# Performance work log

Measured on AMD Instinct MI355X. Metric: run time of the kernel, lower is better.

## Reference

```python
import jax, jax.numpy as jnp
import numpy as np

H = 1024   # hidden_size
IN = 512   # input_size
B = 256    # batch
T = 256    # timesteps

DT = 0.1
DELTA_T = 1.0
Z_MIN = 0.001
Z_MAX = 0.1


def setup_inputs() -> dict:
    key = jax.random.key(0)
    ks = jax.random.split(key, 10)
    bound = 1.0 / np.sqrt(H)
    u = lambda k, shape: jax.random.uniform(k, shape, jnp.float32, -bound, bound)
    return {
        "x":   jax.random.normal(ks[0], (T, IN, B), jnp.float32),
        "c_x": u(ks[1], (H, 1)),
        "c_u": u(ks[2], (H, 1)),
        "c_U": u(ks[3], (H, 1)),
        "w_r": u(ks[4], (H, H)),
        "p_r": u(ks[5], (H, IN)),
        "b_r": u(ks[6], (H, 1)),
        "g_z": u(ks[7], (H, 1)),
        "K":   u(ks[8], (H, H)),
        "p_z": u(ks[9], (H, IN)),
    }


def reference(x, c_x, c_u, c_U, w_r, p_r, b_r, g_z, K, p_z):
    # Gate-rate constants (computed once; they don't depend on state)
    z_x = Z_MIN + (Z_MAX - Z_MIN) * jax.nn.sigmoid(c_x)   # (H,1)
    z_u = Z_MIN + (Z_MAX - Z_MIN) * jax.nn.sigmoid(c_u)   # (H,1)
    Ucap = 0.9 * jax.nn.sigmoid(c_U)                      # (H,1)
    Ucap_sg = jax.lax.stop_gradient(Ucap)                 # clamp bound is detached in torch

    def step(carry, xt):
        X, U, v = carry                   # each (H,B); xt: (IN,B)
        r = jax.nn.sigmoid(v)             # r_t from previous v_t
        X_new = z_x + (1.0 - z_x) * X - DELTA_T * U * X * r
        U_new = Ucap * z_u + (1.0 - z_u) * U + DELTA_T * Ucap * (1.0 - U) * r
        U_new = jnp.clip(U_new, Ucap_sg, 1.0)
        z_t = DT * jax.nn.sigmoid(K @ r + p_z @ xt + g_z)
        v_new = (1.0 - z_t) * v + DT * (w_r @ (U_new * X_new * r) + p_r @ xt + b_r)
        return (X_new, U_new, v_new), v_new

    X0 = jnp.ones((H, B), jnp.float32)
    U0 = jnp.full((H, B), 0.9, jnp.float32)
    v0 = jnp.zeros((H, B), jnp.float32)

    (_, _, _), vs = jax.lax.scan(step, (X0, U0, v0), x)
    # return hidden-state trajectory as (T, batch, hidden)
    return jnp.transpose(vs, (0, 2, 1))
```

## Files before the change

### kernel.cpp

```cpp
#include <hip/hip_runtime.h>
#include <hip/hip_bf16.h>

#define Hh 1024
#define INs 512
#define Bb 256
#define Tt 256
#define DT_ 0.1f
#define Z_MIN_ 0.001f
#define Z_MAX_ 0.1f
#define KW (Hh + INs)
#define NB 256

typedef __attribute__((ext_vector_type(8))) short short8;
typedef __attribute__((ext_vector_type(4))) float f32x4;
typedef __attribute__((ext_vector_type(2))) float f32x2;

__device__ __forceinline__ float sigmoidf_(float x) {
    return 1.0f / (1.0f + __expf(-x));
}

__device__ __forceinline__ unsigned short f2bf(float f) {
    union { float f; unsigned u; } v; v.f = f;
    unsigned r = v.u + 0x7FFFu + ((v.u >> 16) & 1u);
    return (unsigned short)(r >> 16);
}

__global__ __launch_bounds__(256) void build_weights(
    const float* __restrict__ Km, const float* __restrict__ p_z,
    const float* __restrict__ w_r, const float* __restrict__ p_r,
    unsigned short* __restrict__ W1, unsigned short* __restrict__ W2) {
    int idx = blockIdx.x * 256 + threadIdx.x;
    int h = idx / KW, k = idx % KW;
    float a = (k < Hh) ? Km[h * Hh + k] : p_z[h * INs + (k - Hh)];
    float b = (k < Hh) ? w_r[h * Hh + k] : p_r[h * INs + (k - Hh)];
    W1[idx] = f2bf(a);
    W2[idx] = f2bf(b);
}

__global__ __launch_bounds__(256) void transpose_x(
    const float* __restrict__ x, unsigned short* __restrict__ xT) {
    __shared__ unsigned short tile[64][65];
    int t = blockIdx.z;
    int i0 = blockIdx.y * 64;
    int b0 = blockIdx.x * 64;
    int c = threadIdx.x & 63, rbase = threadIdx.x >> 6;
    const float* xp = x + (size_t)t * INs * Bb;
#pragma unroll
    for (int r = 0; r < 16; ++r) {
        int row = r * 4 + rbase;
        tile[row][c] = f2bf(xp[(size_t)(i0 + row) * Bb + (b0 + c)]);
    }
    __syncthreads();
    unsigned short* op = xT + (size_t)t * Bb * INs;
#pragma unroll
    for (int r = 0; r < 16; ++r) {
        int brow = r * 4 + rbase;
        op[(size_t)(b0 + brow) * INs + (i0 + c)] = tile[c][brow];
    }
}

__global__ __launch_bounds__(256) void precomp_gates(
    const float* __restrict__ c_x, const float* __restrict__ c_u,
    const float* __restrict__ c_U,
    float* __restrict__ zxv, float* __restrict__ zuv, float* __restrict__ Ucv) {
    int h = blockIdx.x * 256 + threadIdx.x;
    zxv[h] = Z_MIN_ + (Z_MAX_ - Z_MIN_) * sigmoidf_(c_x[h]);
    zuv[h] = Z_MIN_ + (Z_MAX_ - Z_MIN_) * sigmoidf_(c_u[h]);
    Ucv[h] = 0.9f * sigmoidf_(c_U[h]);
}

__global__ __launch_bounds__(256) void init_state(
    const float* __restrict__ zxv, const float* __restrict__ zuv,
    const float* __restrict__ Ucv,
    unsigned short* __restrict__ R0, unsigned short* __restrict__ M0,
    unsigned* __restrict__ bar) {
    int idx = blockIdx.x * 256 + threadIdx.x;
    if (idx < 16) bar[idx * 32] = 0;
    int h = idx & (Hh - 1);
    float zx = zxv[h], zu = zuv[h], Uc = Ucv[h];
    const float r = 0.5f;
    float Xn = zx + (1.0f - zx) - 0.45f;
    float Un = Uc * zu + (1.0f - zu) * 0.9f + Uc * 0.05f;
    Un = fminf(fmaxf(Un, Uc), 1.0f);
    R0[idx] = f2bf(r);
    M0[idx] = f2bf(Un * Xn * r);
}

__global__ __launch_bounds__(512, 1) void persist_kernel(
    const unsigned short* __restrict__ W1, const unsigned short* __restrict__ W2,
    const unsigned short* __restrict__ xT,
    unsigned short* __restrict__ Rb0, unsigned short* __restrict__ Rb1,
    unsigned short* __restrict__ Mb0, unsigned short* __restrict__ Mb1,
    float* __restrict__ out,
    const float* __restrict__ g_z, const float* __restrict__ b_r,
    const float* __restrict__ zxv, const float* __restrict__ zuv,
    const float* __restrict__ Ucv, unsigned* __restrict__ bar) {

    const int tid = threadIdx.x;
    const int wave = tid >> 6, lane = tid & 63;
    const int m = lane & 15, q = lane >> 4;
    const int kq = wave;
    const int rowg = blockIdx.x >> 4;
    const int colg = blockIdx.x & 15;

    unsigned* cnt = bar + (unsigned)colg * 32;

    const int krec = kq * 128;
    const int kx = kq * 64;
    const int bcol = colg * 16 + m;

    short8 wf1[4][6], wf2[4][6];
#pragma unroll
    for (int rs = 0; rs < 4; ++rs) {
        const int arow = rowg * 64 + rs * 16 + m;
        const unsigned short* w1r = W1 + (size_t)arow * KW + krec + q * 8;
        const unsigned short* w2r = W2 + (size_t)arow * KW + krec + q * 8;
#pragma unroll
        for (int c = 0; c < 4; ++c) {
            wf1[rs][c] = *(const short8*)(w1r + c * 32);
            wf2[rs][c] = *(const short8*)(w2r + c * 32);
        }
        const unsigned short* w1x = W1 + (size_t)arow * KW + Hh + kx + q * 8;
        const unsigned short* w2x = W2 + (size_t)arow * KW + Hh + kx + q * 8;
#pragma unroll
        for (int c = 0; c < 2; ++c) {
            wf1[rs][4 + c] = *(const short8*)(w1x + c * 32);
            wf2[rs][4 + c] = *(const short8*)(w2x + c * 32);
        }
    }

    const int rs_e = wave >> 1, eh = wave & 1;
    const int h2 = rowg * 64 + rs_e * 16 + q * 4 + eh * 2;
    const int bcol_e = colg * 16 + m;

    f32x2 zx2 = *(const f32x2*)(zxv + h2);
    f32x2 zu2 = *(const f32x2*)(zuv + h2);
    f32x2 Uc2 = *(const f32x2*)(Ucv + h2);
    f32x2 gz2 = *(const f32x2*)(g_z + h2);
    f32x2 br2 = *(const f32x2*)(b_r + h2);

    f32x2 vr, Xr, Ur;
#pragma unroll
    for (int j = 0; j < 2; ++j) {
        vr[j] = 0.0f;
        float Xn = zx2[j] + (1.0f - zx2[j]) - 0.45f;
        float Un = Uc2[j] * zu2[j] + (1.0f - zu2[j]) * 0.9f + Uc2[j] * 0.05f;
        Un = fminf(fmaxf(Un, Uc2[j]), 1.0f);
        Xr[j] = Xn; Ur[j] = Un;
    }

    __shared__ f32x4 red[8][4][2][64];

    short8 xb[2];
    {
        const unsigned short* xp = xT + (size_t)bcol * INs + kx + q * 8;
#pragma unroll
        for (int c = 0; c < 2; ++c)
            xb[c] = *(const short8*)(xp + c * 32);
    }

    for (int t = 0; t < Tt; ++t) {
        const unsigned short* Rt = (t & 1) ? Rb1 : Rb0;
        const unsigned short* Mt = (t & 1) ? Mb1 : Mb0;
        unsigned short* Rn = (t & 1) ? Rb0 : Rb1;
        unsigned short* Mn = (t & 1) ? Mb0 : Mb1;

        f32x4 acc[4][2];
#pragma unroll
        for (int rs = 0; rs < 4; ++rs)
#pragma unroll
            for (int mt = 0; mt < 2; ++mt)
                acc[rs][mt] = (f32x4){0.0f, 0.0f, 0.0f, 0.0f};

#pragma unroll
        for (int c = 0; c < 2; ++c)
#pragma unroll
            for (int rs = 0; rs < 4; ++rs) {
                acc[rs][0] = __builtin_amdgcn_mfma_f32_16x16x32_bf16(wf1[rs][4 + c], xb[c], acc[rs][0], 0, 0, 0);
                acc[rs][1] = __builtin_amdgcn_mfma_f32_16x16x32_bf16(wf2[rs][4 + c], xb[c], acc[rs][1], 0, 0, 0);
            }

        if (t + 1 < Tt) {
            const unsigned short* xn = xT + (size_t)(t + 1) * Bb * INs
                                     + (size_t)bcol * INs + kx + q * 8;
#pragma unroll
            for (int c = 0; c < 2; ++c)
                xb[c] = *(const short8*)(xn + c * 32);
        }

        const unsigned short* rp = Rt + (size_t)bcol * Hh + krec + q * 8;
        const unsigned short* mp = Mt + (size_t)bcol * Hh + krec + q * 8;

#pragma unroll
        for (int c = 0; c < 4; ++c) {
            short8 bR = *(const short8*)(rp + c * 32);
            short8 bM = *(const short8*)(mp + c * 32);
#pragma unroll
            for (int rs = 0; rs < 4; ++rs) {
                acc[rs][0] = __builtin_amdgcn_mfma_f32_16x16x32_bf16(wf1[rs][c], bR, acc[rs][0], 0, 0, 0);
                acc[rs][1] = __builtin_amdgcn_mfma_f32_16x16x32_bf16(wf2[rs][c], bM, acc[rs][1], 0, 0, 0);
            }
        }

#pragma unroll
        for (int rs = 0; rs < 4; ++rs)
#pragma unroll
            for (int mt = 0; mt < 2; ++mt)
                red[kq][rs][mt][lane] = acc[rs][mt];
        __syncthreads();

        {
            f32x2 g1 = {0.0f, 0.0f}, g2 = {0.0f, 0.0f};
#pragma unroll
            for (int k2 = 0; k2 < 8; ++k2) {
                const float* p1 = (const float*)&red[k2][rs_e][0][lane];
                const float* p2 = (const float*)&red[k2][rs_e][1][lane];
                g1 += *(const f32x2*)(p1 + eh * 2);
                g2 += *(const f32x2*)(p2 + eh * 2);
            }

            f32x2 vv;
            ushort2 rq, mq;
#pragma unroll
            for (int j = 0; j < 2; ++j) {
                float z = DT_ * sigmoidf_(g1[j] + gz2[j]);
                float vnew = (1.0f - z) * vr[j] + DT_ * (g2[j] + br2[j]);
                vr[j] = vnew;
                vv[j] = vnew;
                float r = sigmoidf_(vnew);
                float Xs = Xr[j], Us = Ur[j];
                float Xn = zx2[j] + (1.0f - zx2[j]) * Xs - Us * Xs * r;
                float Un = Uc2[j] * zu2[j] + (1.0f - zu2[j]) * Us
                         + Uc2[j] * (1.0f - Us) * r;
                Un = fminf(fmaxf(Un, Uc2[j]), 1.0f);
                Xr[j] = Xn; Ur[j] = Un;
                unsigned short rb = f2bf(r), mb = f2bf(Un * Xn * r);
                if (j == 0) { rq.x = rb; mq.x = mb; }
                else        { rq.y = rb; mq.y = mb; }
            }
            const size_t base = (size_t)bcol_e * Hh + h2;
            *(f32x2*)(out + (size_t)t * Bb * Hh + base) = vv;
            *(ushort2*)(Rn + base) = rq;
            *(ushort2*)(Mn + base) = mq;
        }
        __syncthreads();

        if (t + 1 < Tt) {
            if (tid == 0)
                __hip_atomic_fetch_add(cnt, 1u, __ATOMIC_RELAXED,
                                       __HIP_MEMORY_SCOPE_AGENT);
            if (tid == 0) {
                const unsigned tgt = (unsigned)(t + 1) * 16u;
                while (__hip_atomic_load(cnt, __ATOMIC_RELAXED,
                                         __HIP_MEMORY_SCOPE_AGENT) < tgt)
                    __builtin_amdgcn_s_sleep(1);
                asm volatile("buffer_inv sc0" ::: "memory");
            }
            __syncthreads();
        }
    }
}

extern "C" void kernel_launch(void* const* d_in, const int* in_sizes, int n_in,
                              void* d_out, int out_size, void* d_ws, size_t ws_size,
                              hipStream_t stream) {
    const float* x   = (const float*)d_in[0];
    const float* c_x = (const float*)d_in[1];
    const float* c_u = (const float*)d_in[2];
    const float* c_U = (const float*)d_in[3];
    const float* w_r = (const float*)d_in[4];
    const float* p_r = (const float*)d_in[5];
    const float* b_r = (const float*)d_in[6];
    const float* g_z = (const float*)d_in[7];
    const float* Km  = (const float*)d_in[8];
    const float* p_z = (const float*)d_in[9];
    float* out = (float*)d_out;

    char* w = (char*)d_ws;
    unsigned short* W1 = (unsigned short*)w;   w += (size_t)Hh * KW * 2;
    unsigned short* W2 = (unsigned short*)w;   w += (size_t)Hh * KW * 2;
    unsigned short* xT = (unsigned short*)w;   w += (size_t)Tt * Bb * INs * 2;
    unsigned short* Rb0 = (unsigned short*)w;  w += (size_t)Bb * Hh * 2;
    unsigned short* Rb1 = (unsigned short*)w;  w += (size_t)Bb * Hh * 2;
    unsigned short* Mb0 = (unsigned short*)w;  w += (size_t)Bb * Hh * 2;
    unsigned short* Mb1 = (unsigned short*)w;  w += (size_t)Bb * Hh * 2;
    float* zxv = (float*)w;                    w += 4096;
    float* zuv = (float*)w;                    w += 4096;
    float* Ucv = (float*)w;                    w += 4096;
    unsigned* bar = (unsigned*)w;              w += 4096;

    build_weights<<<(Hh * KW) / 256, 256, 0, stream>>>(Km, p_z, w_r, p_r, W1, W2);
    transpose_x<<<dim3(Bb / 64, INs / 64, Tt), 256, 0, stream>>>(x, xT);
    precomp_gates<<<Hh / 256, 256, 0, stream>>>(c_x, c_u, c_U, zxv, zuv, Ucv);
    init_state<<<(Bb * Hh) / 256, 256, 0, stream>>>(zxv, zuv, Ucv, Rb0, Mb0, bar);

    persist_kernel<<<NB, 512, 0, stream>>>(
        W1, W2, xT, Rb0, Rb1, Mb0, Mb1, out,
        g_z, b_r, zxv, zuv, Ucv, bar);
}
```

Measured before the change: 1.884 ms.

## Replace atomic counter barrier with per-block byte flags and restructure epilogue

The per-column-group counter barrier built on atomic adds becomes a set of 16 byte flags, one per row group, each set with a plain atomic store. Waiters poll two 64-bit words and test with a SWAR trick that no byte still holds the old step value. This removes contended read-modify-write traffic on one counter. The R/M operand loads are also hoisted to the top of the step ahead of the x-projection MFMAs to hide latency, and the epilogue now runs on 4 waves with 4-wide vectors instead of 8 waves with 2-wide ones. The risks are that byte flags wrap after 256 steps and that a flag store may become visible before the data stores, since there is no release fence.

```diff
diff --git a/kernel.cpp b/kernel.cpp
--- a/kernel.cpp
+++ b/kernel.cpp
@@ -13,7 +13,6 @@
 
 typedef __attribute__((ext_vector_type(8))) short short8;
 typedef __attribute__((ext_vector_type(4))) float f32x4;
-typedef __attribute__((ext_vector_type(2))) float f32x2;
 
 __device__ __forceinline__ float sigmoidf_(float x) {
     return 1.0f / (1.0f + __expf(-x));
@@ -75,7 +74,7 @@
     unsigned short* __restrict__ R0, unsigned short* __restrict__ M0,
     unsigned* __restrict__ bar) {
     int idx = blockIdx.x * 256 + threadIdx.x;
-    if (idx < 16) bar[idx * 32] = 0;
+    if (idx < 512) bar[idx] = 0;
     int h = idx & (Hh - 1);
     float zx = zxv[h], zu = zuv[h], Uc = Ucv[h];
     const float r = 0.5f;
@@ -103,7 +102,7 @@
     const int rowg = blockIdx.x >> 4;
     const int colg = blockIdx.x & 15;
 
-    unsigned* cnt = bar + (unsigned)colg * 32;
+    unsigned char* flg = (unsigned char*)bar + (unsigned)colg * 128;
 
     const int krec = kq * 128;
     const int kx = kq * 64;
@@ -129,24 +128,24 @@
         }
     }
 
-    const int rs_e = wave >> 1, eh = wave & 1;
-    const int h2 = rowg * 64 + rs_e * 16 + q * 4 + eh * 2;
+    const int rs_e = wave & 3;
+    const int h04 = rowg * 64 + rs_e * 16 + q * 4;
     const int bcol_e = colg * 16 + m;
 
-    f32x2 zx2 = *(const f32x2*)(zxv + h2);
-    f32x2 zu2 = *(const f32x2*)(zuv + h2);
-    f32x2 Uc2 = *(const f32x2*)(Ucv + h2);
-    f32x2 gz2 = *(const f32x2*)(g_z + h2);
-    f32x2 br2 = *(const f32x2*)(b_r + h2);
-
-    f32x2 vr, Xr, Ur;
-#pragma unroll
-    for (int j = 0; j < 2; ++j) {
-        vr[j] = 0.0f;
-        float Xn = zx2[j] + (1.0f - zx2[j]) - 0.45f;
-        float Un = Uc2[j] * zu2[j] + (1.0f - zu2[j]) * 0.9f + Uc2[j] * 0.05f;
-        Un = fminf(fmaxf(Un, Uc2[j]), 1.0f);
-        Xr[j] = Xn; Ur[j] = Un;
+    f32x4 zx4 = *(const f32x4*)(zxv + h04);
+    f32x4 zu4 = *(const f32x4*)(zuv + h04);
+    f32x4 Uc4 = *(const f32x4*)(Ucv + h04);
+    f32x4 gz4 = *(const f32x4*)(g_z + h04);
+    f32x4 br4 = *(const f32x4*)(b_r + h04);
+
+    f32x4 vr, Xr, Ur;
+#pragma unroll
+    for (int e = 0; e < 4; ++e) {
+        vr[e] = 0.0f;
+        float Xn = zx4[e] + (1.0f - zx4[e]) - 0.45f;
+        float Un = Uc4[e] * zu4[e] + (1.0f - zu4[e]) * 0.9f + Uc4[e] * 0.05f;
+        Un = fminf(fmaxf(Un, Uc4[e]), 1.0f);
+        Xr[e] = Xn; Ur[e] = Un;
     }
 
     __shared__ f32x4 red[8][4][2][64];
@@ -165,6 +164,15 @@
         unsigned short* Rn = (t & 1) ? Rb0 : Rb1;
         unsigned short* Mn = (t & 1) ? Mb0 : Mb1;
 
+        const unsigned short* rp = Rt + (size_t)bcol * Hh + krec + q * 8;
+        const unsigned short* mp = Mt + (size_t)bcol * Hh + krec + q * 8;
+        short8 bR[4], bM[4];
+#pragma unroll
+        for (int c = 0; c < 4; ++c) {
+            bR[c] = *(const short8*)(rp + c * 32);
+            bM[c] = *(const short8*)(mp + c * 32);
+        }
+
         f32x4 acc[4][2];
 #pragma unroll
         for (int rs = 0; rs < 4; ++rs)
@@ -188,19 +196,13 @@
                 xb[c] = *(const short8*)(xn + c * 32);
         }
 
-        const unsigned short* rp = Rt + (size_t)bcol * Hh + krec + q * 8;
-        const unsigned short* mp = Mt + (size_t)bcol * Hh + krec + q * 8;
-
-#pragma unroll
-        for (int c = 0; c < 4; ++c) {
-            short8 bR = *(const short8*)(rp + c * 32);
-            short8 bM = *(const short8*)(mp + c * 32);
+#pragma unroll
+        for (int c = 0; c < 4; ++c)
 #pragma unroll
             for (int rs = 0; rs < 4; ++rs) {
-                acc[rs][0] = __builtin_amdgcn_mfma_f32_16x16x32_bf16(wf1[rs][c], bR, acc[rs][0], 0, 0, 0);
-                acc[rs][1] = __builtin_amdgcn_mfma_f32_16x16x32_bf16(wf2[rs][c], bM, acc[rs][1], 0, 0, 0);
-            }
-        }
+                acc[rs][0] = __builtin_amdgcn_mfma_f32_16x16x32_bf16(wf1[rs][c], bR[c], acc[rs][0], 0, 0, 0);
+                acc[rs][1] = __builtin_amdgcn_mfma_f32_16x16x32_bf16(wf2[rs][c], bM[c], acc[rs][1], 0, 0, 0);
+            }
 
 #pragma unroll
         for (int rs = 0; rs < 4; ++rs)
@@ -209,51 +211,63 @@
                 red[kq][rs][mt][lane] = acc[rs][mt];
         __syncthreads();
 
-        {
-            f32x2 g1 = {0.0f, 0.0f}, g2 = {0.0f, 0.0f};
-#pragma unroll
-            for (int k2 = 0; k2 < 8; ++k2) {
-                const float* p1 = (const float*)&red[k2][rs_e][0][lane];
-                const float* p2 = (const float*)&red[k2][rs_e][1][lane];
-                g1 += *(const f32x2*)(p1 + eh * 2);
-                g2 += *(const f32x2*)(p2 + eh * 2);
-            }
-
-            f32x2 vv;
-            ushort2 rq, mq;
-#pragma unroll
-            for (int j = 0; j < 2; ++j) {
-                float z = DT_ * sigmoidf_(g1[j] + gz2[j]);
-                float vnew = (1.0f - z) * vr[j] + DT_ * (g2[j] + br2[j]);
-                vr[j] = vnew;
-                vv[j] = vnew;
+        if (wave < 4) {
+            f32x4 g1 = red[0][rs_e][0][lane];
+            f32x4 g2 = red[0][rs_e][1][lane];
+#pragma unroll
+            for (int k2 = 1; k2 < 8; ++k2) {
+                g1 += red[k2][rs_e][0][lane];
+                g2 += red[k2][rs_e][1][lane];
+            }
+
+            f32x4 vv;
+            ushort4 rq, mq;
+#pragma unroll
+            for (int e = 0; e < 4; ++e) {
+                float z = DT_ * sigmoidf_(g1[e] + gz4[e]);
+                float vnew = (1.0f - z) * vr[e] + DT_ * (g2[e] + br4[e]);
+                vr[e] = vnew;
+                vv[e] = vnew;
                 float r = sigmoidf_(vnew);
-                float Xs = Xr[j], Us = Ur[j];
-                float Xn = zx2[j] + (1.0f - zx2[j]) * Xs - Us * Xs * r;
-                float Un = Uc2[j] * zu2[j] + (1.0f - zu2[j]) * Us
-                         + Uc2[j] * (1.0f - Us) * r;
-                Un = fminf(fmaxf(Un, Uc2[j]), 1.0f);
-                Xr[j] = Xn; Ur[j] = Un;
+                float Xs = Xr[e], Us = Ur[e];
+                float Xn = zx4[e] + (1.0f - zx4[e]) * Xs - Us * Xs * r;
+                float Un = Uc4[e] * zu4[e] + (1.0f - zu4[e]) * Us
+                         + Uc4[e] * (1.0f - Us) * r;
+                Un = fminf(fmaxf(Un, Uc4[e]), 1.0f);
+                Xr[e] = Xn; Ur[e] = Un;
                 unsigned short rb = f2bf(r), mb = f2bf(Un * Xn * r);
-                if (j == 0) { rq.x = rb; mq.x = mb; }
-                else        { rq.y = rb; mq.y = mb; }
-            }
-            const size_t base = (size_t)bcol_e * Hh + h2;
-            *(f32x2*)(out + (size_t)t * Bb * Hh + base) = vv;
-            *(ushort2*)(Rn + base) = rq;
-            *(ushort2*)(Mn + base) = mq;
+                if (e == 0) { rq.x = rb; mq.x = mb; }
+                else if (e == 1) { rq.y = rb; mq.y = mb; }
+                else if (e == 2) { rq.z = rb; mq.z = mb; }
+                else { rq.w = rb; mq.w = mb; }
+            }
+            const size_t base = (size_t)bcol_e * Hh + h04;
+            *(f32x4*)(out + (size_t)t * Bb * Hh + base) = vv;
+            *(ushort4*)(Rn + base) = rq;
+            *(ushort4*)(Mn + base) = mq;
         }
         __syncthreads();
 
         if (t + 1 < Tt) {
-            if (tid == 0)
-                __hip_atomic_fetch_add(cnt, 1u, __ATOMIC_RELAXED,
-                                       __HIP_MEMORY_SCOPE_AGENT);
             if (tid == 0) {
-                const unsigned tgt = (unsigned)(t + 1) * 16u;
-                while (__hip_atomic_load(cnt, __ATOMIC_RELAXED,
-                                         __HIP_MEMORY_SCOPE_AGENT) < tgt)
+                __hip_atomic_store(flg + rowg, (unsigned char)(t + 1),
+                                   __ATOMIC_RELAXED, __HIP_MEMORY_SCOPE_AGENT);
+                const unsigned long long* f64 =
+                    (const unsigned long long*)flg;
+                const unsigned long long low = 0x0101010101010101ull;
+                const unsigned long long hib = 0x8080808080808080ull;
+                const unsigned long long pat = low * (unsigned char)t;
+                for (;;) {
+                    unsigned long long a = __hip_atomic_load(
+                        f64, __ATOMIC_RELAXED, __HIP_MEMORY_SCOPE_AGENT);
+                    unsigned long long b = __hip_atomic_load(
+                        f64 + 1, __ATOMIC_RELAXED, __HIP_MEMORY_SCOPE_AGENT);
+                    unsigned long long xa = a ^ pat, xb2 = b ^ pat;
+                    unsigned long long za = (xa - low) & ~xa & hib;
+                    unsigned long long zb = (xb2 - low) & ~xb2 & hib;
+                    if ((za | zb) == 0ull) break;
                     __builtin_amdgcn_s_sleep(1);
+                }
                 asm volatile("buffer_inv sc0" ::: "memory");
             }
             __syncthreads();
```

Measured after the change: 3.244 ms. 72.2% more time.
